# Kernel optimization log

Measured on AMD Instinct MI355X. Metric: run time of the kernel, lower is better.

The kernel has to match this reference:

```python
import jax, jax.numpy as jnp
import numpy as np
import math

B, N, D, O, H = 8, 1024, 512, 512, 8
HD = O // H  # head_dim = 64


def setup_inputs() -> dict:
    key = jax.random.key(0)
    ks = jax.random.split(key, 12)
    x = jax.random.normal(ks[0], (B, N, D), dtype=jnp.float32)
    adj = jax.random.uniform(ks[1], (B, N, N), dtype=jnp.float32)  # unused by forward math
    mask = jax.random.randint(ks[2], (B, N), 0, 2) > 0  # bool padding mask
    # learned params (torch nn.Linear: y = x @ W.T + b)
    qkv_w = jax.random.normal(ks[3], (3 * O, D), dtype=jnp.float32) / math.sqrt(D)
    qkv_b = jnp.zeros((3 * O,), dtype=jnp.float32)
    # self_loop_W: 1/head_dim + U(0,1), per head, non-trainable
    self_loop_W = (1.0 / HD + jax.random.uniform(ks[4], (1, H, 1, 1))).astype(jnp.float32)
    w1 = jax.random.normal(ks[5], (O, O), dtype=jnp.float32) / math.sqrt(O)
    b1 = jnp.zeros((O,), dtype=jnp.float32)
    w2 = jax.random.normal(ks[6], (O, O), dtype=jnp.float32) / math.sqrt(O)
    b2 = jnp.zeros((O,), dtype=jnp.float32)
    wr = jax.random.normal(ks[7], (O, D), dtype=jnp.float32) / math.sqrt(D)
    br = jnp.zeros((O,), dtype=jnp.float32)
    return {"x": x, "adj": adj, "mask": mask, "self_loop_W": self_loop_W,
            "qkv_w": qkv_w, "qkv_b": qkv_b, "w1": w1, "b1": b1,
            "w2": w2, "b2": b2, "wr": wr, "br": br}


def reference(x, adj, mask, self_loop_W, qkv_w, qkv_b, w1, b1, w2, b2, wr, br):
    fmask = mask.astype(x.dtype)  # [B,N]
    # --- MoireAttention ---
    qkv = x @ qkv_w.T + qkv_b                       # [B,N,3O]
    qkv = qkv.reshape(B, N, 3, H, HD).transpose(2, 0, 3, 1, 4)  # [3,B,H,N,hd]
    Q, K, V = qkv[0], qkv[1], qkv[2]
    scores = jnp.einsum('bhnd,bhmd->bhnm', Q, K) / math.sqrt(HD)  # [B,H,N,N]
    eye = jnp.eye(N, dtype=scores.dtype)
    scores = scores + eye[None, None] * self_loop_W  # per-head diagonal self-loop bias
    mask2d = mask[:, None, :, None] & mask[:, None, None, :]  # [B,1,N,N]
    scores = jnp.where(mask2d, scores, jnp.asarray(-1e6, scores.dtype))
    attn = jax.nn.softmax(scores, axis=-1)
    h = jnp.einsum('bhnm,bhmd->bhnd', attn, V)      # [B,H,N,hd]
    h = h.transpose(0, 2, 1, 3).reshape(B, N, O)
    # --- mask, FFN (eval mode: noise/dropout are identity), mask ---
    h = h * fmask[..., None]
    h = jax.nn.relu(h @ w1.T + b1) @ w2.T + b2
    h = h * fmask[..., None]
    # --- residual blend ---
    x_proj = x @ wr.T + br
    return h * 0.5 + x_proj * 0.5
```

## Files before the change

### kernel.cpp

```cpp
#include <hip/hip_runtime.h>
#include <hip/hip_bf16.h>

typedef __attribute__((ext_vector_type(8))) short short8;
typedef __attribute__((ext_vector_type(4))) float f32x4;
typedef __attribute__((ext_vector_type(4))) short short4v;

#define BB 8
#define NN 1024
#define DD 512
#define OO 512
#define HH 8
#define HD 64
#define MM (BB * NN)

#define QSC 0.18033688f
#define KSHIFT -11.54156032f
#define KMASKED -30000.0f

#define SEG_N 10
struct ConvArgs {
  const float* src[SEG_N];
  __hip_bfloat16* dst[SEG_N];
  int n4[SEG_N];
};

__global__ void convert_kernel(ConvArgs a) {
  const int t = blockIdx.y;
  const int n4 = a.n4[t];
  const float4* fs = (const float4*)a.src[t];
  short4v* d = (short4v*)a.dst[t];
  for (int i = blockIdx.x * blockDim.x + threadIdx.x; i < n4;
       i += gridDim.x * blockDim.x) {
    const float4 v = fs[i];
    union { short4v s; __hip_bfloat16 h[4]; } u;
    u.h[0] = __float2bfloat16(v.x);
    u.h[1] = __float2bfloat16(v.y);
    u.h[2] = __float2bfloat16(v.z);
    u.h[3] = __float2bfloat16(v.w);
    d[i] = u.s;
  }
}

template <int MODE>
__global__ __launch_bounds__(256) void gemm_bt(
    const __hip_bfloat16* __restrict__ A0, const __hip_bfloat16* __restrict__ B0,
    const __hip_bfloat16* __restrict__ A1, const __hip_bfloat16* __restrict__ B1,
    const __hip_bfloat16* __restrict__ bias0, const __hip_bfloat16* __restrict__ bias1,
    const int* __restrict__ mask,
    __hip_bfloat16* __restrict__ out0, __hip_bfloat16* __restrict__ out1,
    __hip_bfloat16* __restrict__ out2, float* __restrict__ outf,
    int M, int N, int Kd) {
  __shared__ __hip_bfloat16 As[128 * 40];
  __shared__ __hip_bfloat16 Bs[128 * 40];

  const int tid  = threadIdx.x;
  const int wave = tid >> 6;
  const int lane = tid & 63;
  const int fl   = lane & 15;
  const int fk   = (lane >> 4) * 8;
  const int wm   = (wave & 1) * 64;
  const int wn   = (wave >> 1) * 64;
  const int m0   = blockIdx.y * 128;
  const int n0   = blockIdx.x * 128;
  const int srow = tid >> 2;
  const int scol = (tid & 3) * 8;

  f32x4 acc[4][4];
#pragma unroll
  for (int i = 0; i < 4; ++i)
#pragma unroll
    for (int j = 0; j < 4; ++j) acc[i][j] = (f32x4){0.f, 0.f, 0.f, 0.f};

  const int npairs = (MODE == 2) ? 2 : 1;
  for (int p = 0; p < npairs; ++p) {
    const __hip_bfloat16* Ap = (p == 0) ? A0 : A1;
    const __hip_bfloat16* Bp = (p == 0) ? B0 : B1;
    for (int k0 = 0; k0 < Kd; k0 += 32) {
      __syncthreads();
      uint4 av0 = *(const uint4*)(Ap + (size_t)(m0 + srow) * Kd + k0 + scol);
      uint4 av1 = *(const uint4*)(Ap + (size_t)(m0 + srow + 64) * Kd + k0 + scol);
      uint4 bv0 = *(const uint4*)(Bp + (size_t)(n0 + srow) * Kd + k0 + scol);
      uint4 bv1 = *(const uint4*)(Bp + (size_t)(n0 + srow + 64) * Kd + k0 + scol);
      *(uint4*)&As[srow * 40 + scol] = av0;
      *(uint4*)&As[(srow + 64) * 40 + scol] = av1;
      *(uint4*)&Bs[srow * 40 + scol] = bv0;
      *(uint4*)&Bs[(srow + 64) * 40 + scol] = bv1;
      __syncthreads();

      short8 af[4], bfr[4];
#pragma unroll
      for (int i = 0; i < 4; ++i)
        af[i] = *(const short8*)&As[(wm + i * 16 + fl) * 40 + fk];
#pragma unroll
      for (int j = 0; j < 4; ++j)
        bfr[j] = *(const short8*)&Bs[(wn + j * 16 + fl) * 40 + fk];
#pragma unroll
      for (int i = 0; i < 4; ++i)
#pragma unroll
        for (int j = 0; j < 4; ++j)
          acc[i][j] = __builtin_amdgcn_mfma_f32_16x16x32_bf16(af[i], bfr[j],
                                                              acc[i][j], 0, 0, 0);
    }
  }

  const int rb = (lane >> 4) * 4;

  if (MODE == 0) {
    const int part = n0 >> 9;
    if (part < 2) {
      __hip_bfloat16* dst = (part == 0) ? out0 : out1;
      const float sc = (part == 0) ? QSC : 1.0f;
#pragma unroll
      for (int j = 0; j < 4; ++j) {
        const int colb  = n0 + wn + j * 16;
        const int o     = colb & 511;
        const int headq = o >> 6;
        const int d     = (o & 63) + fl;
        const float bi  = __bfloat162float(bias0[colb + fl]);
#pragma unroll
        for (int i = 0; i < 4; ++i) {
#pragma unroll
          for (int r = 0; r < 4; ++r) {
            const int row = m0 + wm + i * 16 + rb + r;
            const int bb  = row >> 10;
            const int nn  = row & 1023;
            dst[((size_t)((bb << 3) + headq) * NN + nn) * HD + d] =
                __float2bfloat16((acc[i][j][r] + bi) * sc);
          }
        }
      }
    } else {
      __syncthreads();
      __hip_bfloat16* tsc = As + wave * 1120;
      const int bb  = (m0 + wm) >> 10;
      const int nnb = (m0 + wm) & 1023;
      const int dl  = lane >> 2;
      const int cc  = (lane & 3) * 16;
#pragma unroll
      for (int j = 0; j < 4; ++j) {
        const int colb  = n0 + wn + j * 16;
        const int o     = colb & 511;
        const int headq = o >> 6;
        const int dbase = o & 63;
        const float bi  = __bfloat162float(bias0[colb + fl]);
#pragma unroll
        for (int i = 0; i < 4; ++i) {
#pragma unroll
          for (int r = 0; r < 4; ++r) {
            const int rr = i * 16 + rb + r;
            tsc[fl * 70 + rr] = __float2bfloat16(acc[i][j][r] + bi);
          }
        }
        uint4 r0 = *(const uint4*)&tsc[dl * 70 + cc];
        uint4 r1 = *(const uint4*)&tsc[dl * 70 + cc + 8];
        __hip_bfloat16* vdst =
            out2 + ((size_t)((bb << 3) + headq) * HD + dbase + dl) * NN + nnb;
        *(uint4*)&vdst[cc] = r0;
        *(uint4*)&vdst[cc + 8] = r1;
      }
    }
  } else if (MODE == 1) {
#pragma unroll
    for (int j = 0; j < 4; ++j) {
      const int col  = n0 + wn + j * 16 + fl;
      const float bi = __bfloat162float(bias0[col]);
#pragma unroll
      for (int i = 0; i < 4; ++i) {
#pragma unroll
        for (int r = 0; r < 4; ++r) {
          const int row = m0 + wm + i * 16 + rb + r;
          float v = fmaxf(acc[i][j][r] + bi, 0.f);
          if (mask[row] == 0) v = 0.f;
          out0[(size_t)row * N + col] = __float2bfloat16(v);
        }
      }
    }
  } else {
#pragma unroll
    for (int j = 0; j < 4; ++j) {
      const int col   = n0 + wn + j * 16 + fl;
      const float b2v = __bfloat162float(bias0[col]);
      const float brv = __bfloat162float(bias1[col]);
#pragma unroll
      for (int i = 0; i < 4; ++i) {
#pragma unroll
        for (int r = 0; r < 4; ++r) {
          const int row = m0 + wm + i * 16 + rb + r;
          const float v = acc[i][j][r] + brv + (mask[row] != 0 ? b2v : 0.f);
          outf[(size_t)row * N + col] = 0.5f * v;
        }
      }
    }
  }
}

__global__ __launch_bounds__(256) void attn_kernel(
    const __hip_bfloat16* __restrict__ Qb, const __hip_bfloat16* __restrict__ Kb,
    const __hip_bfloat16* __restrict__ Vt, const __hip_bfloat16* __restrict__ slw,
    const int* __restrict__ mask, __hip_bfloat16* __restrict__ hb) {
  __shared__ __hip_bfloat16 Qs[64 * 72];
  __shared__ __hip_bfloat16 Ks[64 * 72];
  __shared__ __hip_bfloat16 Vs[64 * 72];
  __shared__ __hip_bfloat16 Ps[64 * 72];
  __shared__ float Msf[NN];

  const int tid  = threadIdx.x;
  const int wave = tid >> 6;
  const int lane = tid & 63;
  const int fl   = lane & 15;
  const int fk   = (lane >> 4) * 8;
  const int rb   = (lane >> 4) * 4;
  const int bh   = blockIdx.x >> 4;
  const int qblk = blockIdx.x & 15;
  const int b    = bh >> 3;
  const int head = bh & 7;
  const int q0   = qblk * 64;

  const float slwL2 = __bfloat162float(slw[head]) * 1.44269504f;

  const int srow = tid >> 2;
  const int sc   = (tid & 3) * 8;
  {
    const __hip_bfloat16* qg = Qb + ((size_t)bh * NN + q0) * HD;
    uint4 v0 = *(const uint4*)(qg + srow * HD + sc);
    uint4 v1 = *(const uint4*)(qg + srow * HD + sc + 32);
    *(uint4*)&Qs[srow * 72 + sc] = v0;
    *(uint4*)&Qs[srow * 72 + sc + 32] = v1;
#pragma unroll
    for (int k = 0; k < 4; ++k) {
      const int idx = tid * 4 + k;
      Msf[idx] = (mask[b * NN + idx] != 0) ? KSHIFT : KMASKED;
    }
  }
  __syncthreads();
  const short8 qa0 = *(const short8*)&Qs[(wave * 16 + fl) * 72 + fk];
  const short8 qa1 = *(const short8*)&Qs[(wave * 16 + fl) * 72 + fk + 32];

  float lsum[4] = {0.f, 0.f, 0.f, 0.f};
  f32x4 Oacc[4];
#pragma unroll
  for (int t = 0; t < 4; ++t) Oacc[t] = (f32x4){0.f, 0.f, 0.f, 0.f};

  for (int kb = 0; kb < NN / 64; ++kb) {
    const int kbase = kb * 64;
    __syncthreads();
    {
      const __hip_bfloat16* kg = Kb + ((size_t)bh * NN + kbase) * HD;
      uint4 v0 = *(const uint4*)(kg + srow * HD + sc);
      uint4 v1 = *(const uint4*)(kg + srow * HD + sc + 32);
      *(uint4*)&Ks[srow * 72 + sc] = v0;
      *(uint4*)&Ks[srow * 72 + sc + 32] = v1;
      const __hip_bfloat16* vg = Vt + ((size_t)bh * HD + srow) * NN + kbase;
      uint4 w0 = *(const uint4*)(vg + sc);
      uint4 w1 = *(const uint4*)(vg + sc + 32);
      *(uint4*)&Vs[srow * 72 + sc] = w0;
      *(uint4*)&Vs[srow * 72 + sc + 32] = w1;
    }
    __syncthreads();

    f32x4 sfr[4];
#pragma unroll
    for (int j = 0; j < 4; ++j) {
      const short8 kf0 = *(const short8*)&Ks[(j * 16 + fl) * 72 + fk];
      const short8 kf1 = *(const short8*)&Ks[(j * 16 + fl) * 72 + fk + 32];
      f32x4 z = (f32x4){0.f, 0.f, 0.f, 0.f};
      z = __builtin_amdgcn_mfma_f32_16x16x32_bf16(qa0, kf0, z, 0, 0, 0);
      z = __builtin_amdgcn_mfma_f32_16x16x32_bf16(qa1, kf1, z, 0, 0, 0);
      sfr[j] = z;
    }

    float mb[4];
#pragma unroll
    for (int j = 0; j < 4; ++j) mb[j] = Msf[kbase + j * 16 + fl];

    if (kb != qblk) {
#pragma unroll
      for (int r = 0; r < 4; ++r) {
        const int qrow_l = wave * 16 + rb + r;
#pragma unroll
        for (int j = 0; j < 4; ++j) {
          const float pv = exp2f(sfr[j][r] + mb[j]);
          lsum[r] += pv;
          Ps[qrow_l * 72 + j * 16 + fl] = __float2bfloat16(pv);
        }
      }
    } else {
#pragma unroll
      for (int r = 0; r < 4; ++r) {
        const int qrow_l = wave * 16 + rb + r;
#pragma unroll
        for (int j = 0; j < 4; ++j) {
          float sv = sfr[j][r] + mb[j];
          if (j * 16 + fl == qrow_l) sv += slwL2;
          const float pv = exp2f(sv);
          lsum[r] += pv;
          Ps[qrow_l * 72 + j * 16 + fl] = __float2bfloat16(pv);
        }
      }
    }

    const short8 pa0 = *(const short8*)&Ps[(wave * 16 + fl) * 72 + fk];
    const short8 pa1 = *(const short8*)&Ps[(wave * 16 + fl) * 72 + fk + 32];
#pragma unroll
    for (int t = 0; t < 4; ++t) {
      const short8 vf0 = *(const short8*)&Vs[(t * 16 + fl) * 72 + fk];
      const short8 vf1 = *(const short8*)&Vs[(t * 16 + fl) * 72 + fk + 32];
      Oacc[t] = __builtin_amdgcn_mfma_f32_16x16x32_bf16(pa0, vf0, Oacc[t], 0, 0, 0);
      Oacc[t] = __builtin_amdgcn_mfma_f32_16x16x32_bf16(pa1, vf1, Oacc[t], 0, 0, 0);
    }
  }

  float scl[4];
#pragma unroll
  for (int r = 0; r < 4; ++r) {
    float l = lsum[r];
#pragma unroll
    for (int off = 1; off < 16; off <<= 1) l += __shfl_xor(l, off, 64);
    const int qrow_g = q0 + wave * 16 + rb + r;
    const float qm = (mask[b * NN + qrow_g] != 0) ? 1.f : 0.f;
    scl[r] = qm / fmaxf(l, 1e-30f);
  }
#pragma unroll
  for (int t = 0; t < 4; ++t) {
    const int d = t * 16 + fl;
#pragma unroll
    for (int r = 0; r < 4; ++r) {
      const int qrow_g = q0 + wave * 16 + rb + r;
      hb[(size_t)(b * NN + qrow_g) * OO + head * HD + d] =
          __float2bfloat16(Oacc[t][r] * scl[r]);
    }
  }
}

extern "C" void kernel_launch(void* const* d_in, const int* in_sizes, int n_in,
                              void* d_out, int out_size, void* d_ws, size_t ws_size,
                              hipStream_t stream) {
  const float* x_raw    = (const float*)d_in[0];
  const int* mask       = (const int*)d_in[2];
  const float* slw_raw  = (const float*)d_in[3];
  const float* qkvw_raw = (const float*)d_in[4];
  const float* qkvb_raw = (const float*)d_in[5];
  const float* w1_raw   = (const float*)d_in[6];
  const float* b1_raw   = (const float*)d_in[7];
  const float* w2_raw   = (const float*)d_in[8];
  const float* b2_raw   = (const float*)d_in[9];
  const float* wr_raw   = (const float*)d_in[10];
  const float* br_raw   = (const float*)d_in[11];
  float* outf           = (float*)d_out;

  __hip_bfloat16* p = (__hip_bfloat16*)d_ws;
  __hip_bfloat16* xc    = p; p += (size_t)MM * DD;
  __hip_bfloat16* qkvwc = p; p += 3 * OO * DD;
  __hip_bfloat16* w1c   = p; p += OO * OO;
  __hip_bfloat16* w2c   = p; p += OO * OO;
  __hip_bfloat16* wrc   = p; p += OO * DD;
  __hip_bfloat16* qkvbc = p; p += 3 * OO;
  __hip_bfloat16* b1c   = p; p += OO;
  __hip_bfloat16* b2c   = p; p += OO;
  __hip_bfloat16* brc   = p; p += OO;
  __hip_bfloat16* slwc  = p; p += 64;
  const size_t ebuf = (size_t)BB * HH * NN * HD;
  __hip_bfloat16* Qb = p; p += ebuf;
  __hip_bfloat16* Kb = p; p += ebuf;
  __hip_bfloat16* Vb = p; p += ebuf;
  __hip_bfloat16* hb = (__hip_bfloat16*)d_out;
  __hip_bfloat16* tb = Kb;

  if (ws_size < (size_t)((char*)p - (char*)d_ws)) return;

  ConvArgs ca;
  ca.src[0] = x_raw;    ca.dst[0] = xc;    ca.n4[0] = MM * DD / 4;
  ca.src[1] = qkvw_raw; ca.dst[1] = qkvwc; ca.n4[1] = 3 * OO * DD / 4;
  ca.src[2] = w1_raw;   ca.dst[2] = w1c;   ca.n4[2] = OO * OO / 4;
  ca.src[3] = w2_raw;   ca.dst[3] = w2c;   ca.n4[3] = OO * OO / 4;
  ca.src[4] = wr_raw;   ca.dst[4] = wrc;   ca.n4[4] = OO * DD / 4;
  ca.src[5] = qkvb_raw; ca.dst[5] = qkvbc; ca.n4[5] = 3 * OO / 4;
  ca.src[6] = b1_raw;   ca.dst[6] = b1c;   ca.n4[6] = OO / 4;
  ca.src[7] = b2_raw;   ca.dst[7] = b2c;   ca.n4[7] = OO / 4;
  ca.src[8] = br_raw;   ca.dst[8] = brc;   ca.n4[8] = OO / 4;
  ca.src[9] = slw_raw;  ca.dst[9] = slwc;  ca.n4[9] = HH / 4;
  convert_kernel<<<dim3(128, SEG_N), 256, 0, stream>>>(ca);

  gemm_bt<0><<<dim3(3 * OO / 128, MM / 128), 256, 0, stream>>>(
      xc, qkvwc, nullptr, nullptr, qkvbc, nullptr, mask, Qb, Kb, Vb, nullptr,
      MM, 3 * OO, DD);
  attn_kernel<<<BB * HH * (NN / 64), 256, 0, stream>>>(Qb, Kb, Vb, slwc, mask, hb);
  gemm_bt<1><<<dim3(OO / 128, MM / 128), 256, 0, stream>>>(
      hb, w1c, nullptr, nullptr, b1c, nullptr, mask, tb, nullptr, nullptr, nullptr,
      MM, OO, OO);
  gemm_bt<2><<<dim3(OO / 128, MM / 128), 256, 0, stream>>>(
      tb, w2c, xc, wrc, b2c, brc, mask, nullptr, nullptr, nullptr, outf,
      MM, OO, DD);
}
```

Baseline: 231.0 us.

## Use 64x64 tiles for FFN GEMMs and transpose score MFMA in attention

Splits the QKV GEMM into its own kernel and gives the two FFN/residual GEMMs 64x64 tiles, so their grids grow from 256 to 1024 blocks and fill the GPU's compute units better. In attention, the score MFMA operands are swapped so each lane holds four consecutive key columns of one query row. That allows vectorized mask loads, packed 4-element P stores to shared memory and a cheaper row-sum reduction with fewer shuffles. The attention block index is also reordered so the 64 batch-head pairs vary fastest across blocks. Smaller GEMM tiles lower per-block data reuse and add global traffic.

New measurement: 232.8 us. About the same (+0.8%).

```diff
diff --git a/kernel.cpp b/kernel.cpp
--- a/kernel.cpp
+++ b/kernel.cpp
@@ -41,15 +41,11 @@
   }
 }
 
-template <int MODE>
-__global__ __launch_bounds__(256) void gemm_bt(
+__global__ __launch_bounds__(256) void gemm_qkv(
     const __hip_bfloat16* __restrict__ A0, const __hip_bfloat16* __restrict__ B0,
-    const __hip_bfloat16* __restrict__ A1, const __hip_bfloat16* __restrict__ B1,
-    const __hip_bfloat16* __restrict__ bias0, const __hip_bfloat16* __restrict__ bias1,
-    const int* __restrict__ mask,
+    const __hip_bfloat16* __restrict__ bias0,
     __hip_bfloat16* __restrict__ out0, __hip_bfloat16* __restrict__ out1,
-    __hip_bfloat16* __restrict__ out2, float* __restrict__ outf,
-    int M, int N, int Kd) {
+    __hip_bfloat16* __restrict__ out2, int Kd) {
   __shared__ __hip_bfloat16 As[128 * 40];
   __shared__ __hip_bfloat16 Bs[128 * 40];
 
@@ -71,101 +67,154 @@
 #pragma unroll
     for (int j = 0; j < 4; ++j) acc[i][j] = (f32x4){0.f, 0.f, 0.f, 0.f};
 
+  for (int k0 = 0; k0 < Kd; k0 += 32) {
+    __syncthreads();
+    uint4 av0 = *(const uint4*)(A0 + (size_t)(m0 + srow) * Kd + k0 + scol);
+    uint4 av1 = *(const uint4*)(A0 + (size_t)(m0 + srow + 64) * Kd + k0 + scol);
+    uint4 bv0 = *(const uint4*)(B0 + (size_t)(n0 + srow) * Kd + k0 + scol);
+    uint4 bv1 = *(const uint4*)(B0 + (size_t)(n0 + srow + 64) * Kd + k0 + scol);
+    *(uint4*)&As[srow * 40 + scol] = av0;
+    *(uint4*)&As[(srow + 64) * 40 + scol] = av1;
+    *(uint4*)&Bs[srow * 40 + scol] = bv0;
+    *(uint4*)&Bs[(srow + 64) * 40 + scol] = bv1;
+    __syncthreads();
+
+    short8 af[4], bfr[4];
+#pragma unroll
+    for (int i = 0; i < 4; ++i)
+      af[i] = *(const short8*)&As[(wm + i * 16 + fl) * 40 + fk];
+#pragma unroll
+    for (int j = 0; j < 4; ++j)
+      bfr[j] = *(const short8*)&Bs[(wn + j * 16 + fl) * 40 + fk];
+#pragma unroll
+    for (int i = 0; i < 4; ++i)
+#pragma unroll
+      for (int j = 0; j < 4; ++j)
+        acc[i][j] = __builtin_amdgcn_mfma_f32_16x16x32_bf16(af[i], bfr[j],
+                                                            acc[i][j], 0, 0, 0);
+  }
+
+  const int rb = (lane >> 4) * 4;
+  const int part = n0 >> 9;
+  if (part < 2) {
+    __hip_bfloat16* dst = (part == 0) ? out0 : out1;
+    const float sc = (part == 0) ? QSC : 1.0f;
+#pragma unroll
+    for (int j = 0; j < 4; ++j) {
+      const int colb  = n0 + wn + j * 16;
+      const int o     = colb & 511;
+      const int headq = o >> 6;
+      const int d     = (o & 63) + fl;
+      const float bi  = __bfloat162float(bias0[colb + fl]);
+#pragma unroll
+      for (int i = 0; i < 4; ++i) {
+#pragma unroll
+        for (int r = 0; r < 4; ++r) {
+          const int row = m0 + wm + i * 16 + rb + r;
+          const int bb  = row >> 10;
+          const int nn  = row & 1023;
+          dst[((size_t)((bb << 3) + headq) * NN + nn) * HD + d] =
+              __float2bfloat16((acc[i][j][r] + bi) * sc);
+        }
+      }
+    }
+  } else {
+    __syncthreads();
+    __hip_bfloat16* tsc = As + wave * 1120;
+    const int bb  = (m0 + wm) >> 10;
+    const int nnb = (m0 + wm) & 1023;
+    const int dl  = lane >> 2;
+    const int cc  = (lane & 3) * 16;
+#pragma unroll
+    for (int j = 0; j < 4; ++j) {
+      const int colb  = n0 + wn + j * 16;
+      const int o     = colb & 511;
+      const int headq = o >> 6;
+      const int dbase = o & 63;
+      const float bi  = __bfloat162float(bias0[colb + fl]);
+#pragma unroll
+      for (int i = 0; i < 4; ++i) {
+#pragma unroll
+        for (int r = 0; r < 4; ++r) {
+          const int rr = i * 16 + rb + r;
+          tsc[fl * 70 + rr] = __float2bfloat16(acc[i][j][r] + bi);
+        }
+      }
+      uint4 r0 = *(const uint4*)&tsc[dl * 70 + cc];
+      uint4 r1 = *(const uint4*)&tsc[dl * 70 + cc + 8];
+      __hip_bfloat16* vdst =
+          out2 + ((size_t)((bb << 3) + headq) * HD + dbase + dl) * NN + nnb;
+      *(uint4*)&vdst[cc] = r0;
+      *(uint4*)&vdst[cc + 8] = r1;
+    }
+  }
+}
+
+template <int MODE>
+__global__ __launch_bounds__(256) void gemm64(
+    const __hip_bfloat16* __restrict__ A0, const __hip_bfloat16* __restrict__ B0,
+    const __hip_bfloat16* __restrict__ A1, const __hip_bfloat16* __restrict__ B1,
+    const __hip_bfloat16* __restrict__ bias0, const __hip_bfloat16* __restrict__ bias1,
+    const int* __restrict__ mask,
+    __hip_bfloat16* __restrict__ out0, float* __restrict__ outf,
+    int N, int Kd) {
+  __shared__ __hip_bfloat16 As[64 * 40];
+  __shared__ __hip_bfloat16 Bs[64 * 40];
+
+  const int tid  = threadIdx.x;
+  const int wave = tid >> 6;
+  const int lane = tid & 63;
+  const int fl   = lane & 15;
+  const int fk   = (lane >> 4) * 8;
+  const int wm   = (wave & 1) * 32;
+  const int wn   = (wave >> 1) * 32;
+  const int m0   = blockIdx.y * 64;
+  const int n0   = blockIdx.x * 64;
+  const int srow = tid >> 2;
+  const int scol = (tid & 3) * 8;
+
+  f32x4 acc[2][2];
+#pragma unroll
+  for (int i = 0; i < 2; ++i)
+#pragma unroll
+    for (int j = 0; j < 2; ++j) acc[i][j] = (f32x4){0.f, 0.f, 0.f, 0.f};
+
   const int npairs = (MODE == 2) ? 2 : 1;
   for (int p = 0; p < npairs; ++p) {
     const __hip_bfloat16* Ap = (p == 0) ? A0 : A1;
     const __hip_bfloat16* Bp = (p == 0) ? B0 : B1;
     for (int k0 = 0; k0 < Kd; k0 += 32) {
       __syncthreads();
-      uint4 av0 = *(const uint4*)(Ap + (size_t)(m0 + srow) * Kd + k0 + scol);
-      uint4 av1 = *(const uint4*)(Ap + (size_t)(m0 + srow + 64) * Kd + k0 + scol);
-      uint4 bv0 = *(const uint4*)(Bp + (size_t)(n0 + srow) * Kd + k0 + scol);
-      uint4 bv1 = *(const uint4*)(Bp + (size_t)(n0 + srow + 64) * Kd + k0 + scol);
-      *(uint4*)&As[srow * 40 + scol] = av0;
-      *(uint4*)&As[(srow + 64) * 40 + scol] = av1;
-      *(uint4*)&Bs[srow * 40 + scol] = bv0;
-      *(uint4*)&Bs[(srow + 64) * 40 + scol] = bv1;
+      uint4 av = *(const uint4*)(Ap + (size_t)(m0 + srow) * Kd + k0 + scol);
+      uint4 bv = *(const uint4*)(Bp + (size_t)(n0 + srow) * Kd + k0 + scol);
+      *(uint4*)&As[srow * 40 + scol] = av;
+      *(uint4*)&Bs[srow * 40 + scol] = bv;
       __syncthreads();
 
-      short8 af[4], bfr[4];
-#pragma unroll
-      for (int i = 0; i < 4; ++i)
+      short8 af[2], bfr[2];
+#pragma unroll
+      for (int i = 0; i < 2; ++i)
         af[i] = *(const short8*)&As[(wm + i * 16 + fl) * 40 + fk];
 #pragma unroll
-      for (int j = 0; j < 4; ++j)
+      for (int j = 0; j < 2; ++j)
         bfr[j] = *(const short8*)&Bs[(wn + j * 16 + fl) * 40 + fk];
 #pragma unroll
-      for (int i = 0; i < 4; ++i)
-#pragma unroll
-        for (int j = 0; j < 4; ++j)
+      for (int i = 0; i < 2; ++i)
+#pragma unroll
+        for (int j = 0; j < 2; ++j)
           acc[i][j] = __builtin_amdgcn_mfma_f32_16x16x32_bf16(af[i], bfr[j],
                                                               acc[i][j], 0, 0, 0);
     }
   }
 
   const int rb = (lane >> 4) * 4;
-
-  if (MODE == 0) {
-    const int part = n0 >> 9;
-    if (part < 2) {
-      __hip_bfloat16* dst = (part == 0) ? out0 : out1;
-      const float sc = (part == 0) ? QSC : 1.0f;
-#pragma unroll
-      for (int j = 0; j < 4; ++j) {
-        const int colb  = n0 + wn + j * 16;
-        const int o     = colb & 511;
-        const int headq = o >> 6;
-        const int d     = (o & 63) + fl;
-        const float bi  = __bfloat162float(bias0[colb + fl]);
-#pragma unroll
-        for (int i = 0; i < 4; ++i) {
-#pragma unroll
-          for (int r = 0; r < 4; ++r) {
-            const int row = m0 + wm + i * 16 + rb + r;
-            const int bb  = row >> 10;
-            const int nn  = row & 1023;
-            dst[((size_t)((bb << 3) + headq) * NN + nn) * HD + d] =
-                __float2bfloat16((acc[i][j][r] + bi) * sc);
-          }
-        }
-      }
-    } else {
-      __syncthreads();
-      __hip_bfloat16* tsc = As + wave * 1120;
-      const int bb  = (m0 + wm) >> 10;
-      const int nnb = (m0 + wm) & 1023;
-      const int dl  = lane >> 2;
-      const int cc  = (lane & 3) * 16;
-#pragma unroll
-      for (int j = 0; j < 4; ++j) {
-        const int colb  = n0 + wn + j * 16;
-        const int o     = colb & 511;
-        const int headq = o >> 6;
-        const int dbase = o & 63;
-        const float bi  = __bfloat162float(bias0[colb + fl]);
-#pragma unroll
-        for (int i = 0; i < 4; ++i) {
-#pragma unroll
-          for (int r = 0; r < 4; ++r) {
-            const int rr = i * 16 + rb + r;
-            tsc[fl * 70 + rr] = __float2bfloat16(acc[i][j][r] + bi);
-          }
-        }
-        uint4 r0 = *(const uint4*)&tsc[dl * 70 + cc];
-        uint4 r1 = *(const uint4*)&tsc[dl * 70 + cc + 8];
-        __hip_bfloat16* vdst =
-            out2 + ((size_t)((bb << 3) + headq) * HD + dbase + dl) * NN + nnb;
-        *(uint4*)&vdst[cc] = r0;
-        *(uint4*)&vdst[cc + 8] = r1;
-      }
-    }
-  } else if (MODE == 1) {
-#pragma unroll
-    for (int j = 0; j < 4; ++j) {
+  if (MODE == 1) {
+#pragma unroll
+    for (int j = 0; j < 2; ++j) {
       const int col  = n0 + wn + j * 16 + fl;
       const float bi = __bfloat162float(bias0[col]);
 #pragma unroll
-      for (int i = 0; i < 4; ++i) {
+      for (int i = 0; i < 2; ++i) {
 #pragma unroll
         for (int r = 0; r < 4; ++r) {
           const int row = m0 + wm + i * 16 + rb + r;
@@ -177,12 +226,12 @@
     }
   } else {
 #pragma unroll
-    for (int j = 0; j < 4; ++j) {
+    for (int j = 0; j < 2; ++j) {
       const int col   = n0 + wn + j * 16 + fl;
       const float b2v = __bfloat162float(bias0[col]);
       const float brv = __bfloat162float(bias1[col]);
 #pragma unroll
-      for (int i = 0; i < 4; ++i) {
+      for (int i = 0; i < 2; ++i) {
 #pragma unroll
         for (int r = 0; r < 4; ++r) {
           const int row = m0 + wm + i * 16 + rb + r;
@@ -208,10 +257,11 @@
   const int wave = tid >> 6;
   const int lane = tid & 63;
   const int fl   = lane & 15;
-  const int fk   = (lane >> 4) * 8;
-  const int rb   = (lane >> 4) * 4;
-  const int bh   = blockIdx.x >> 4;
-  const int qblk = blockIdx.x & 15;
+  const int quad = lane >> 4;
+  const int fk   = quad * 8;
+  const int rb   = quad * 4;
+  const int bh   = blockIdx.x & 63;
+  const int qblk = blockIdx.x >> 6;
   const int b    = bh >> 3;
   const int head = bh & 7;
   const int q0   = qblk * 64;
@@ -236,7 +286,7 @@
   const short8 qa0 = *(const short8*)&Qs[(wave * 16 + fl) * 72 + fk];
   const short8 qa1 = *(const short8*)&Qs[(wave * 16 + fl) * 72 + fk + 32];
 
-  float lsum[4] = {0.f, 0.f, 0.f, 0.f};
+  float lsum = 0.f;
   f32x4 Oacc[4];
 #pragma unroll
   for (int t = 0; t < 4; ++t) Oacc[t] = (f32x4){0.f, 0.f, 0.f, 0.f};
@@ -264,39 +314,28 @@
       const short8 kf0 = *(const short8*)&Ks[(j * 16 + fl) * 72 + fk];
       const short8 kf1 = *(const short8*)&Ks[(j * 16 + fl) * 72 + fk + 32];
       f32x4 z = (f32x4){0.f, 0.f, 0.f, 0.f};
-      z = __builtin_amdgcn_mfma_f32_16x16x32_bf16(qa0, kf0, z, 0, 0, 0);
-      z = __builtin_amdgcn_mfma_f32_16x16x32_bf16(qa1, kf1, z, 0, 0, 0);
+      z = __builtin_amdgcn_mfma_f32_16x16x32_bf16(kf0, qa0, z, 0, 0, 0);
+      z = __builtin_amdgcn_mfma_f32_16x16x32_bf16(kf1, qa1, z, 0, 0, 0);
       sfr[j] = z;
     }
 
-    float mb[4];
-#pragma unroll
-    for (int j = 0; j < 4; ++j) mb[j] = Msf[kbase + j * 16 + fl];
-
-    if (kb != qblk) {
-#pragma unroll
-      for (int r = 0; r < 4; ++r) {
-        const int qrow_l = wave * 16 + rb + r;
-#pragma unroll
-        for (int j = 0; j < 4; ++j) {
-          const float pv = exp2f(sfr[j][r] + mb[j]);
-          lsum[r] += pv;
-          Ps[qrow_l * 72 + j * 16 + fl] = __float2bfloat16(pv);
-        }
+    if (kb == qblk) {
+      if ((fl >> 2) == quad) sfr[wave][fl & 3] += slwL2;
+    }
+
+#pragma unroll
+    for (int j = 0; j < 4; ++j) {
+      const f32x4 mb4 = *(const f32x4*)&Msf[kbase + j * 16 + quad * 4];
+      union { short4v s; __hip_bfloat16 h[4]; } pu;
+      float ps = 0.f;
+#pragma unroll
+      for (int e = 0; e < 4; ++e) {
+        const float pv = exp2f(sfr[j][e] + mb4[e]);
+        ps += pv;
+        pu.h[e] = __float2bfloat16(pv);
       }
-    } else {
-#pragma unroll
-      for (int r = 0; r < 4; ++r) {
-        const int qrow_l = wave * 16 + rb + r;
-#pragma unroll
-        for (int j = 0; j < 4; ++j) {
-          float sv = sfr[j][r] + mb[j];
-          if (j * 16 + fl == qrow_l) sv += slwL2;
-          const float pv = exp2f(sv);
-          lsum[r] += pv;
-          Ps[qrow_l * 72 + j * 16 + fl] = __float2bfloat16(pv);
-        }
-      }
+      lsum += ps;
+      *(short4v*)&Ps[(wave * 16 + fl) * 72 + j * 16 + quad * 4] = pu.s;
     }
 
     const short8 pa0 = *(const short8*)&Ps[(wave * 16 + fl) * 72 + fk];
@@ -310,16 +349,17 @@
     }
   }
 
+  float l = lsum;
+  l += __shfl_xor(l, 16, 64);
+  l += __shfl_xor(l, 32, 64);
+  const int qrow_me = q0 + wave * 16 + fl;
+  const float qm = (mask[b * NN + qrow_me] != 0) ? 1.f : 0.f;
+  const float sf = qm / fmaxf(l, 1e-30f);
+
   float scl[4];
 #pragma unroll
-  for (int r = 0; r < 4; ++r) {
-    float l = lsum[r];
-#pragma unroll
-    for (int off = 1; off < 16; off <<= 1) l += __shfl_xor(l, off, 64);
-    const int qrow_g = q0 + wave * 16 + rb + r;
-    const float qm = (mask[b * NN + qrow_g] != 0) ? 1.f : 0.f;
-    scl[r] = qm / fmaxf(l, 1e-30f);
-  }
+  for (int r = 0; r < 4; ++r) scl[r] = __shfl(sf, rb + r, 64);
+
 #pragma unroll
   for (int t = 0; t < 4; ++t) {
     const int d = t * 16 + fl;
@@ -381,14 +421,11 @@
   ca.src[9] = slw_raw;  ca.dst[9] = slwc;  ca.n4[9] = HH / 4;
   convert_kernel<<<dim3(128, SEG_N), 256, 0, stream>>>(ca);
 
-  gemm_bt<0><<<dim3(3 * OO / 128, MM / 128), 256, 0, stream>>>(
-      xc, qkvwc, nullptr, nullptr, qkvbc, nullptr, mask, Qb, Kb, Vb, nullptr,
-      MM, 3 * OO, DD);
+  gemm_qkv<<<dim3(3 * OO / 128, MM / 128), 256, 0, stream>>>(
+      xc, qkvwc, qkvbc, Qb, Kb, Vb, DD);
   attn_kernel<<<BB * HH * (NN / 64), 256, 0, stream>>>(Qb, Kb, Vb, slwc, mask, hb);
-  gemm_bt<1><<<dim3(OO / 128, MM / 128), 256, 0, stream>>>(
-      hb, w1c, nullptr, nullptr, b1c, nullptr, mask, tb, nullptr, nullptr, nullptr,
-      MM, OO, OO);
-  gemm_bt<2><<<dim3(OO / 128, MM / 128), 256, 0, stream>>>(
-      tb, w2c, xc, wrc, b2c, brc, mask, nullptr, nullptr, nullptr, outf,
-      MM, OO, DD);
+  gemm64<1><<<dim3(OO / 64, MM / 64), 256, 0, stream>>>(
+      hb, w1c, nullptr, nullptr, b1c, nullptr, mask, tb, nullptr, OO, OO);
+  gemm64<2><<<dim3(OO / 64, MM / 64), 256, 0, stream>>>(
+      tb, w2c, xc, wrc, b2c, brc, mask, nullptr, outf, OO, DD);
 }
```
